# Optimization experiments

Measured on AMD Instinct MI355X. Metric: run time of the kernel, lower is better.

The kernel has to match this reference:

```python
import jax, jax.numpy as jnp
import numpy as np

B, SEQ, D = 2, 1024, 768
E, H = 8, 3072          # num_experts, expert hidden (mlp_ratio=4)
CAPACITY = 2            # k = CAPACITY * num_tokens


def setup_inputs() -> dict:
    key = jax.random.key(0)
    ks = jax.random.split(key, 6)
    x = jax.random.normal(ks[0], (B, SEQ, D), dtype=jnp.float32)
    gate_weight = jax.random.normal(ks[1], (E, D), dtype=jnp.float32) * 0.006
    w1 = jax.random.normal(ks[2], (E, D, H), dtype=jnp.float32) * (1.0 / np.sqrt(D))
    b1 = jnp.zeros((E, H), dtype=jnp.float32)
    w2 = jax.random.normal(ks[3], (E, H, D), dtype=jnp.float32) * (1.0 / np.sqrt(H))
    b2 = jnp.zeros((E, D), dtype=jnp.float32)
    return {"x": x, "gate_weight": gate_weight, "w1": w1, "b1": b1, "w2": w2, "b2": b2}


def reference(x, gate_weight, w1, b1, w2, b2):
    Bb, s, d = x.shape
    xf = x.reshape(-1, d)                     # [S, D]
    S = xf.shape[0]
    k = S * CAPACITY
    logits = xf @ gate_weight.T               # [S, E]
    scores = jax.nn.softmax(logits, axis=-1).T  # [E, S]
    # flattened top-k over all (expert, token) pairs -> sparse gate matrix
    vals, idx = jax.lax.top_k(scores.reshape(-1), k)
    gate = jnp.zeros((E * S,), dtype=x.dtype).at[idx].add(vals).reshape(E, S)
    # expert MLPs (GELU-tanh) applied per expert; zero gate entries kill
    # non-routed (expert, token) pairs -> same math as gather/MLP/scatter.
    h = jax.nn.gelu(jnp.einsum('sd,edh->esh', xf, w1) + b1[:, None, :], approximate=True)
    out = jnp.einsum('esh,ehd->esd', h, w2) + b2[:, None, :]   # [E, S, D]
    y = jnp.einsum('es,esd->sd', gate, out)    # weighted combine + sum over experts
    return y.reshape(Bb, s, d)
```

## Files before the change

kernel.cpp:

```cpp
#include <hip/hip_runtime.h>
#include <math.h>

#define S_TOK 2048
#define NEXP  8
#define DDIM  768
#define HDIM  3072
#define KSEL  4096

typedef __attribute__((ext_vector_type(8))) short short8;
typedef __attribute__((ext_vector_type(4))) float f32x4;

__device__ __forceinline__ unsigned short f2bf(float f) {
  unsigned u = __float_as_uint(f);
  u += 0x7fffu + ((u >> 16) & 1u);
  return (unsigned short)(u >> 16);
}

__device__ __forceinline__ float gelu_fast(float v) {
  float u = 0.7978845608028654f * (v + 0.044715f * v * v * v);
  float t = __expf(-2.0f * fabsf(u));
  float th = (1.0f - t) / (1.0f + t);
  th = copysignf(th, u);
  return 0.5f * v * (1.0f + th);
}

__global__ __launch_bounds__(256) void zero_kernel(float* __restrict__ p, int n) {
  int i = blockIdx.x * 256 + threadIdx.x;
  if (i < n) p[i] = 0.f;
}

__global__ __launch_bounds__(256) void convx_kernel(const float* __restrict__ x,
                                                    short* __restrict__ xb) {
  int i = (blockIdx.x * 256 + threadIdx.x) * 8;
  float4 a = *(const float4*)(x + i);
  float4 b = *(const float4*)(x + i + 4);
  short8 v;
  v[0] = (short)f2bf(a.x); v[1] = (short)f2bf(a.y);
  v[2] = (short)f2bf(a.z); v[3] = (short)f2bf(a.w);
  v[4] = (short)f2bf(b.x); v[5] = (short)f2bf(b.y);
  v[6] = (short)f2bf(b.z); v[7] = (short)f2bf(b.w);
  *(short8*)(xb + i) = v;
}

__global__ __launch_bounds__(256) void gate_kernel(
    const float* __restrict__ x, const float* __restrict__ gw,
    float* __restrict__ scores)
{
  int tid  = threadIdx.x;
  int lane = tid & 63;
  int wid  = tid >> 6;
  int token = blockIdx.x * 4 + wid;
  const float* xr = x + (size_t)token * DDIM;

  float acc[NEXP];
#pragma unroll
  for (int e = 0; e < NEXP; ++e) acc[e] = 0.f;

  for (int d = lane; d < DDIM; d += 64) {
    float xv = xr[d];
#pragma unroll
    for (int e = 0; e < NEXP; ++e) acc[e] += xv * gw[e * DDIM + d];
  }
#pragma unroll
  for (int e = 0; e < NEXP; ++e) {
    for (int off = 32; off; off >>= 1) acc[e] += __shfl_down(acc[e], off, 64);
  }
  if (lane == 0) {
    float m = acc[0];
#pragma unroll
    for (int e = 1; e < NEXP; ++e) m = fmaxf(m, acc[e]);
    float p[NEXP], s = 0.f;
#pragma unroll
    for (int e = 0; e < NEXP; ++e) { p[e] = expf(acc[e] - m); s += p[e]; }
    float inv = 1.0f / s;
#pragma unroll
    for (int e = 0; e < NEXP; ++e) scores[e * S_TOK + token] = p[e] * inv;
  }
}

__device__ unsigned block_scan_excl(unsigned v, volatile unsigned* wsum) {
  int tid = threadIdx.x, lane = tid & 63, wid = tid >> 6;
  __syncthreads();
  unsigned x = v;
#pragma unroll
  for (int off = 1; off < 64; off <<= 1) {
    unsigned t = __shfl_up(x, off, 64);
    if (lane >= off) x += t;
  }
  if (lane == 63) wsum[wid] = x;
  __syncthreads();
  if (tid < 64) {
    unsigned w = (lane < 16) ? wsum[lane] : 0u;
#pragma unroll
    for (int off = 1; off < 16; off <<= 1) {
      unsigned t = __shfl_up(w, off, 64);
      if (lane >= off) w += t;
    }
    if (lane < 16) wsum[lane] = w;
  }
  __syncthreads();
  unsigned woff = (wid > 0) ? wsum[wid - 1] : 0u;
  return woff + (x - v);
}

__global__ __launch_bounds__(1024) void select_kernel(
    const float* __restrict__ scores,
    int* __restrict__ tokenlist, float* __restrict__ slotgate,
    int* __restrict__ offsets)
{
  __shared__ unsigned cnt;
  __shared__ unsigned wsum[16];
  int tid = threadIdx.x;
  int base = tid * 16;

  float sv[16]; unsigned key[16];
#pragma unroll
  for (int j = 0; j < 16; ++j) {
    sv[j] = scores[base + j];
    key[j] = __float_as_uint(sv[j]);
  }

  unsigned lo = 0, hi = 0x3F800000u;
  while (lo < hi) {
    unsigned mid = lo + ((hi - lo + 1) >> 1);
    if (tid == 0) cnt = 0;
    __syncthreads();
    unsigned c = 0;
#pragma unroll
    for (int j = 0; j < 16; ++j) c += (key[j] >= mid) ? 1u : 0u;
    for (int off = 32; off; off >>= 1) c += __shfl_down(c, off, 64);
    if ((tid & 63) == 0) atomicAdd(&cnt, c);
    __syncthreads();
    unsigned tot = cnt;
    __syncthreads();
    if (tot >= (unsigned)KSEL) lo = mid; else hi = mid - 1;
  }
  unsigned V = lo;

  if (tid == 0) cnt = 0;
  __syncthreads();
  {
    unsigned c = 0;
#pragma unroll
    for (int j = 0; j < 16; ++j) c += (key[j] > V) ? 1u : 0u;
    for (int off = 32; off; off >>= 1) c += __shfl_down(c, off, 64);
    if ((tid & 63) == 0) atomicAdd(&cnt, c);
  }
  __syncthreads();
  int need = KSEL - (int)cnt;
  __syncthreads();

  unsigned tloc = 0;
#pragma unroll
  for (int j = 0; j < 16; ++j) tloc += (key[j] == V) ? 1u : 0u;
  unsigned texcl = block_scan_excl(tloc, wsum);

  unsigned selmask = 0, sloc = 0, trun = texcl;
#pragma unroll
  for (int j = 0; j < 16; ++j) {
    bool f;
    if (key[j] > V) f = true;
    else if (key[j] == V) { f = ((int)trun < need); ++trun; }
    else f = false;
    if (f) { selmask |= (1u << j); ++sloc; }
  }
  unsigned sexcl = block_scan_excl(sloc, wsum);

  if ((tid & 127) == 0) offsets[tid >> 7] = (int)sexcl;
  if (tid == 0) offsets[NEXP] = KSEL;

  unsigned p = sexcl;
#pragma unroll
  for (int j = 0; j < 16; ++j) {
    int i = base + j;
    if (selmask & (1u << j)) {
      tokenlist[p] = i & (S_TOK - 1);
      slotgate[p] = sv[j];
      ++p;
    }
  }
}

template <int MODE>
__global__ __launch_bounds__(256) void moe_mfma(
    const short* __restrict__ Abase, const float* __restrict__ W,
    const float* __restrict__ bias, void* __restrict__ outp,
    const int* __restrict__ offsets, const int* __restrict__ tokenlist,
    const float* __restrict__ slotgate)
{
  const int e = (int)blockIdx.x;
  const int K = (MODE == 1) ? DDIM : HDIM;
  const int N = (MODE == 1) ? HDIM : DDIM;
  const int tile  = (MODE == 1) ? (int)blockIdx.z : ((int)blockIdx.z >> 2);
  const int split = (MODE == 1) ? 0 : ((int)blockIdx.z & 3);
  const int klen  = 768;
  const int kb = split * klen;

  const int r0 = offsets[e];
  const int rows = offsets[e + 1] - r0;
  const int rowbase = tile << 7;
  if (rowbase >= rows) return;
  int vr = rows - rowbase; if (vr > 128) vr = 128;
  const int colbase = (int)blockIdx.y << 7;

  __shared__ short As[128 * 40];
  __shared__ short Bb[128 * 40];

  const int tid = threadIdx.x;
  const int lane = tid & 63;
  const int wid = tid >> 6;
  const int wr = (wid >> 1) << 6;
  const int wc = (wid & 1) << 6;
  const int l15 = lane & 15;
  const int lq = lane >> 4;

  const int ar = tid >> 1;
  const int ak = (tid & 1) << 4;
  const short* arow;
  {
    int cr = (ar < vr) ? ar : (vr - 1);
    if (MODE == 1) arow = Abase + (size_t)tokenlist[r0 + rowbase + cr] * DDIM;
    else           arow = Abase + (size_t)(r0 + rowbase + cr) * HDIM + kb;
  }
  const int bn = tid & 127;
  const int bk = (tid >> 7) << 4;
  const float* wcol = W + (size_t)e * K * N + colbase + bn;

  f32x4 acc[4][4];
#pragma unroll
  for (int i = 0; i < 4; ++i)
#pragma unroll
    for (int j = 0; j < 4; ++j) acc[i][j] = (f32x4){0.f, 0.f, 0.f, 0.f};

  short8 av0, av1;
  float bwA[16], bwB[16];
  {
    const short* ap = arow + ak;
    av0 = *(const short8*)(ap);
    av1 = *(const short8*)(ap + 8);
    const float* wpA = wcol + (size_t)(kb + bk) * N;
    const float* wpB = wcol + (size_t)(kb + 32 + bk) * N;
#pragma unroll
    for (int j = 0; j < 16; ++j) bwA[j] = wpA[(size_t)j * N];
#pragma unroll
    for (int j = 0; j < 16; ++j) bwB[j] = wpB[(size_t)j * N];
  }

#define WRITE_LDS(BW)                                            \
  {                                                              \
    *(short8*)&As[ar * 40 + ak] = av0;                           \
    *(short8*)&As[ar * 40 + ak + 8] = av1;                       \
    short8 b0, b1;                                               \
    _Pragma("unroll")                                            \
    for (int m = 0; m < 8; ++m) {                                \
      b0[m] = (short)f2bf(BW[m]);                                \
      b1[m] = (short)f2bf(BW[m + 8]);                            \
    }                                                            \
    *(short8*)&Bb[bn * 40 + bk] = b0;                            \
    *(short8*)&Bb[bn * 40 + bk + 8] = b1;                        \
  }

#define LOAD_A(KN)                                               \
  {                                                              \
    const short* ap = arow + (KN) + ak;                          \
    av0 = *(const short8*)(ap);                                  \
    av1 = *(const short8*)(ap + 8);                              \
  }

#define LOAD_B(BW, KN)                                           \
  {                                                              \
    const float* wp = wcol + (size_t)(kb + (KN) + bk) * N;       \
    _Pragma("unroll")                                            \
    for (int j = 0; j < 16; ++j) BW[j] = wp[(size_t)j * N];      \
  }

#define FRAG_MFMA()                                              \
  {                                                              \
    short8 af[4], bfr[4];                                        \
    _Pragma("unroll")                                            \
    for (int i = 0; i < 4; ++i)                                  \
      af[i] = *(const short8*)&As[(wr + i * 16 + l15) * 40 + lq * 8]; \
    _Pragma("unroll")                                            \
    for (int j = 0; j < 4; ++j)                                  \
      bfr[j] = *(const short8*)&Bb[(wc + j * 16 + l15) * 40 + lq * 8]; \
    _Pragma("unroll")                                            \
    for (int i = 0; i < 4; ++i)                                  \
      _Pragma("unroll")                                          \
      for (int j = 0; j < 4; ++j)                                \
        acc[i][j] = __builtin_amdgcn_mfma_f32_16x16x32_bf16(af[i], bfr[j], acc[i][j], 0, 0, 0); \
  }

#pragma unroll 1
  for (int k0 = 0; k0 < klen; k0 += 64) {
    __syncthreads();
    WRITE_LDS(bwA);
    __syncthreads();
    LOAD_A(k0 + 32);
    { int kn = k0 + 64; if (kn >= klen) kn = k0; LOAD_B(bwA, kn); }
    FRAG_MFMA();
    __syncthreads();
    WRITE_LDS(bwB);
    __syncthreads();
    { int kn = k0 + 64; if (kn >= klen) kn = k0; LOAD_A(kn); }
    { int kn = k0 + 96; if (kn >= klen) kn = k0; LOAD_B(bwB, kn); }
    FRAG_MFMA();
  }

  if (MODE == 1) {
    short* hb = (short*)outp;
    const float* bp = bias + (size_t)e * N + colbase;
#pragma unroll
    for (int i = 0; i < 4; ++i) {
      int rb = wr + i * 16 + lq * 4;
#pragma unroll
      for (int j = 0; j < 4; ++j) {
        int col = wc + j * 16 + l15;
        float bvv = bp[col];
#pragma unroll
        for (int p = 0; p < 4; ++p) {
          int r = rb + p;
          if (r < vr)
            hb[(size_t)(r0 + rowbase + r) * HDIM + colbase + col] =
                (short)f2bf(gelu_fast(acc[i][j][p] + bvv));
        }
      }
    }
  } else {
    float* y = (float*)outp;
    const float* bp = bias + (size_t)e * N + colbase;
#pragma unroll
    for (int i = 0; i < 4; ++i) {
      int rb = wr + i * 16 + lq * 4;
#pragma unroll
      for (int p = 0; p < 4; ++p) {
        int r = rb + p;
        if (r < vr) {
          int gi = r0 + rowbase + r;
          float g = slotgate[gi];
          float* yrow = y + (size_t)tokenlist[gi] * N + colbase;
#pragma unroll
          for (int j = 0; j < 4; ++j) {
            int col = wc + j * 16 + l15;
            float v = acc[i][j][p] + (split == 0 ? bp[col] : 0.f);
            atomicAdd(&yrow[col], g * v);
          }
        }
      }
    }
  }
}

extern "C" void kernel_launch(void* const* d_in, const int* in_sizes, int n_in,
                              void* d_out, int out_size, void* d_ws, size_t ws_size,
                              hipStream_t stream) {
  const float* x  = (const float*)d_in[0];
  const float* gw = (const float*)d_in[1];
  const float* w1 = (const float*)d_in[2];
  const float* b1 = (const float*)d_in[3];
  const float* w2 = (const float*)d_in[4];
  const float* b2 = (const float*)d_in[5];
  float* y = (float*)d_out;

  char* ws = (char*)d_ws;
  float* scores    = (float*)(ws);
  int*   tokenlist = (int*)(ws + (64 << 10));
  float* slotgate  = (float*)(ws + (80 << 10));
  int*   offsets   = (int*)(ws + (96 << 10));
  short* xbf       = (short*)(ws + (128 << 10));
  short* hbuf      = (short*)(ws + (128 << 10) + (size_t)S_TOK * DDIM * 2);

  zero_kernel<<<(out_size + 255) / 256, 256, 0, stream>>>(y, out_size);
  convx_kernel<<<S_TOK * DDIM / 2048, 256, 0, stream>>>(x, xbf);
  gate_kernel<<<S_TOK / 4, 256, 0, stream>>>(x, gw, scores);
  select_kernel<<<1, 1024, 0, stream>>>(scores, tokenlist, slotgate, offsets);

  dim3 g1(NEXP, HDIM / 128, 16);
  moe_mfma<1><<<g1, 256, 0, stream>>>(xbf, w1, b1, hbuf, offsets, tokenlist, slotgate);
  dim3 g2(NEXP, DDIM / 128, 64);
  moe_mfma<2><<<g2, 256, 0, stream>>>(hbuf, w2, b2, y, offsets, tokenlist, slotgate);
}
```

Measured before the change: 208.2 us.

## Coalesce weight loads with transposed LDS reads and replace atomics with combine pass

Weight tiles are now read as contiguous float4 rows along N rather than strided column gathers. They are stored k-major in LDS and fed to MFMA through ds_read_b64_tr_b16 transposed reads, with the k-step reduced to 32 and a single register buffer. The second GEMM's split-K drops from 4 to 2 and writes partial results to a workspace buffer instead of issuing atomicAdds into y. A new combine kernel uses a posmap produced by the selection kernel to gather and gate-weight those partials, which also removes the zeroing kernel. This trades atomic contention and strided global loads for an extra kernel launch and more intermediate memory traffic.

```diff
diff --git a/kernel.cpp b/kernel.cpp
--- a/kernel.cpp
+++ b/kernel.cpp
@@ -9,6 +9,7 @@
 
 typedef __attribute__((ext_vector_type(8))) short short8;
 typedef __attribute__((ext_vector_type(4))) float f32x4;
+typedef __attribute__((ext_vector_type(2))) unsigned int u32x2;
 
 __device__ __forceinline__ unsigned short f2bf(float f) {
   unsigned u = __float_as_uint(f);
@@ -22,11 +23,6 @@
   float th = (1.0f - t) / (1.0f + t);
   th = copysignf(th, u);
   return 0.5f * v * (1.0f + th);
-}
-
-__global__ __launch_bounds__(256) void zero_kernel(float* __restrict__ p, int n) {
-  int i = blockIdx.x * 256 + threadIdx.x;
-  if (i < n) p[i] = 0.f;
 }
 
 __global__ __launch_bounds__(256) void convx_kernel(const float* __restrict__ x,
@@ -106,7 +102,7 @@
 __global__ __launch_bounds__(1024) void select_kernel(
     const float* __restrict__ scores,
     int* __restrict__ tokenlist, float* __restrict__ slotgate,
-    int* __restrict__ offsets)
+    int* __restrict__ offsets, int* __restrict__ posmap)
 {
   __shared__ unsigned cnt;
   __shared__ unsigned wsum[16];
@@ -174,9 +170,12 @@
   for (int j = 0; j < 16; ++j) {
     int i = base + j;
     if (selmask & (1u << j)) {
+      posmap[i] = (int)p;
       tokenlist[p] = i & (S_TOK - 1);
       slotgate[p] = sv[j];
       ++p;
+    } else {
+      posmap[i] = -1;
     }
   }
 }
@@ -185,15 +184,14 @@
 __global__ __launch_bounds__(256) void moe_mfma(
     const short* __restrict__ Abase, const float* __restrict__ W,
     const float* __restrict__ bias, void* __restrict__ outp,
-    const int* __restrict__ offsets, const int* __restrict__ tokenlist,
-    const float* __restrict__ slotgate)
+    const int* __restrict__ offsets, const int* __restrict__ tokenlist)
 {
   const int e = (int)blockIdx.x;
   const int K = (MODE == 1) ? DDIM : HDIM;
   const int N = (MODE == 1) ? HDIM : DDIM;
-  const int tile  = (MODE == 1) ? (int)blockIdx.z : ((int)blockIdx.z >> 2);
-  const int split = (MODE == 1) ? 0 : ((int)blockIdx.z & 3);
-  const int klen  = 768;
+  const int tile  = (MODE == 1) ? (int)blockIdx.z : ((int)blockIdx.z >> 1);
+  const int split = (MODE == 1) ? 0 : ((int)blockIdx.z & 1);
+  const int klen  = (MODE == 1) ? DDIM : (HDIM / 2);
   const int kb = split * klen;
 
   const int r0 = offsets[e];
@@ -204,7 +202,8 @@
   const int colbase = (int)blockIdx.y << 7;
 
   __shared__ short As[128 * 40];
-  __shared__ short Bb[128 * 40];
+  __shared__ __align__(16) short Bs[32 * 128];
+  const unsigned bs_lds = (unsigned)(uintptr_t)&Bs[0];
 
   const int tid = threadIdx.x;
   const int lane = tid & 63;
@@ -222,9 +221,11 @@
     if (MODE == 1) arow = Abase + (size_t)tokenlist[r0 + rowbase + cr] * DDIM;
     else           arow = Abase + (size_t)(r0 + rowbase + cr) * HDIM + kb;
   }
-  const int bn = tid & 127;
-  const int bk = (tid >> 7) << 4;
-  const float* wcol = W + (size_t)e * K * N + colbase + bn;
+
+  const int sk = tid >> 3;
+  const int g8 = tid & 7;
+  const float* wsrc = W + (size_t)e * K * N + (size_t)kb * N + colbase + g8 * 16;
+  short* bwr = (short*)Bs + ((((sk >> 2) << 3) + g8) << 6) + ((sk & 3) << 4);
 
   f32x4 acc[4][4];
 #pragma unroll
@@ -232,78 +233,57 @@
 #pragma unroll
     for (int j = 0; j < 4; ++j) acc[i][j] = (f32x4){0.f, 0.f, 0.f, 0.f};
 
-  short8 av0, av1;
-  float bwA[16], bwB[16];
+  short8 avA0, avA1;
+  float4 bw[4];
   {
-    const short* ap = arow + ak;
-    av0 = *(const short8*)(ap);
-    av1 = *(const short8*)(ap + 8);
-    const float* wpA = wcol + (size_t)(kb + bk) * N;
-    const float* wpB = wcol + (size_t)(kb + 32 + bk) * N;
-#pragma unroll
-    for (int j = 0; j < 16; ++j) bwA[j] = wpA[(size_t)j * N];
-#pragma unroll
-    for (int j = 0; j < 16; ++j) bwB[j] = wpB[(size_t)j * N];
-  }
-
-#define WRITE_LDS(BW)                                            \
-  {                                                              \
-    *(short8*)&As[ar * 40 + ak] = av0;                           \
-    *(short8*)&As[ar * 40 + ak + 8] = av1;                       \
-    short8 b0, b1;                                               \
-    _Pragma("unroll")                                            \
-    for (int m = 0; m < 8; ++m) {                                \
-      b0[m] = (short)f2bf(BW[m]);                                \
-      b1[m] = (short)f2bf(BW[m + 8]);                            \
-    }                                                            \
-    *(short8*)&Bb[bn * 40 + bk] = b0;                            \
-    *(short8*)&Bb[bn * 40 + bk + 8] = b1;                        \
-  }
-
-#define LOAD_A(KN)                                               \
-  {                                                              \
-    const short* ap = arow + (KN) + ak;                          \
-    av0 = *(const short8*)(ap);                                  \
-    av1 = *(const short8*)(ap + 8);                              \
-  }
-
-#define LOAD_B(BW, KN)                                           \
-  {                                                              \
-    const float* wp = wcol + (size_t)(kb + (KN) + bk) * N;       \
-    _Pragma("unroll")                                            \
-    for (int j = 0; j < 16; ++j) BW[j] = wp[(size_t)j * N];      \
-  }
-
-#define FRAG_MFMA()                                              \
-  {                                                              \
-    short8 af[4], bfr[4];                                        \
-    _Pragma("unroll")                                            \
-    for (int i = 0; i < 4; ++i)                                  \
-      af[i] = *(const short8*)&As[(wr + i * 16 + l15) * 40 + lq * 8]; \
-    _Pragma("unroll")                                            \
-    for (int j = 0; j < 4; ++j)                                  \
-      bfr[j] = *(const short8*)&Bb[(wc + j * 16 + l15) * 40 + lq * 8]; \
-    _Pragma("unroll")                                            \
-    for (int i = 0; i < 4; ++i)                                  \
-      _Pragma("unroll")                                          \
-      for (int j = 0; j < 4; ++j)                                \
-        acc[i][j] = __builtin_amdgcn_mfma_f32_16x16x32_bf16(af[i], bfr[j], acc[i][j], 0, 0, 0); \
+    avA0 = *(const short8*)(arow + ak);
+    avA1 = *(const short8*)(arow + ak + 8);
+    const float* wp = wsrc + (size_t)sk * N;
+#pragma unroll
+    for (int q = 0; q < 4; ++q) bw[q] = *(const float4*)(wp + 4 * q);
   }
 
 #pragma unroll 1
-  for (int k0 = 0; k0 < klen; k0 += 64) {
-    __syncthreads();
-    WRITE_LDS(bwA);
-    __syncthreads();
-    LOAD_A(k0 + 32);
-    { int kn = k0 + 64; if (kn >= klen) kn = k0; LOAD_B(bwA, kn); }
-    FRAG_MFMA();
-    __syncthreads();
-    WRITE_LDS(bwB);
-    __syncthreads();
-    { int kn = k0 + 64; if (kn >= klen) kn = k0; LOAD_A(kn); }
-    { int kn = k0 + 96; if (kn >= klen) kn = k0; LOAD_B(bwB, kn); }
-    FRAG_MFMA();
+  for (int k0 = 0; k0 < klen; k0 += 32) {
+    __syncthreads();
+    *(short8*)&As[ar * 40 + ak] = avA0;
+    *(short8*)&As[ar * 40 + ak + 8] = avA1;
+#pragma unroll
+    for (int q = 0; q < 4; ++q) {
+      u32x2 pk;
+      pk[0] = (unsigned)f2bf(bw[q].x) | ((unsigned)f2bf(bw[q].y) << 16);
+      pk[1] = (unsigned)f2bf(bw[q].z) | ((unsigned)f2bf(bw[q].w) << 16);
+      *(u32x2*)(bwr + 4 * q) = pk;
+    }
+    __syncthreads();
+    if (k0 + 32 < klen) {
+      avA0 = *(const short8*)(arow + k0 + 32 + ak);
+      avA1 = *(const short8*)(arow + k0 + 32 + ak + 8);
+      const float* wp = wsrc + (size_t)(k0 + 32 + sk) * N;
+#pragma unroll
+      for (int q = 0; q < 4; ++q) bw[q] = *(const float4*)(wp + 4 * q);
+    }
+    short8 af[4], bfr[4];
+#pragma unroll
+    for (int i = 0; i < 4; ++i)
+      af[i] = *(const short8*)&As[(wr + i * 16 + l15) * 40 + lq * 8];
+#pragma unroll
+    for (int j = 0; j < 4; ++j) {
+      unsigned off = bs_lds + ((unsigned)((lq << 4) + (wc >> 4) + j) << 7) +
+                     ((unsigned)l15 << 3);
+      union { short8 s; u32x2 u[2]; } fb;
+      asm volatile("ds_read_b64_tr_b16 %0, %2 offset:0\n\t"
+                   "ds_read_b64_tr_b16 %1, %2 offset:1024"
+                   : "=&v"(fb.u[0]), "=&v"(fb.u[1]) : "v"(off));
+      bfr[j] = fb.s;
+    }
+    asm volatile("s_waitcnt lgkmcnt(0)" ::: "memory");
+    __builtin_amdgcn_sched_barrier(0);
+#pragma unroll
+    for (int i = 0; i < 4; ++i)
+#pragma unroll
+      for (int j = 0; j < 4; ++j)
+        acc[i][j] = __builtin_amdgcn_mfma_f32_16x16x32_bf16(af[i], bfr[j], acc[i][j], 0, 0, 0);
   }
 
   if (MODE == 1) {
@@ -326,7 +306,7 @@
       }
     }
   } else {
-    float* y = (float*)outp;
+    float* ob = (float*)outp + (size_t)split * KSEL * DDIM;
     const float* bp = bias + (size_t)e * N + colbase;
 #pragma unroll
     for (int i = 0; i < 4; ++i) {
@@ -335,19 +315,41 @@
       for (int p = 0; p < 4; ++p) {
         int r = rb + p;
         if (r < vr) {
-          int gi = r0 + rowbase + r;
-          float g = slotgate[gi];
-          float* yrow = y + (size_t)tokenlist[gi] * N + colbase;
+          float* orow = ob + (size_t)(r0 + rowbase + r) * DDIM + colbase;
 #pragma unroll
           for (int j = 0; j < 4; ++j) {
             int col = wc + j * 16 + l15;
-            float v = acc[i][j][p] + (split == 0 ? bp[col] : 0.f);
-            atomicAdd(&yrow[col], g * v);
+            orow[col] = acc[i][j][p] + (split == 0 ? bp[col] : 0.f);
           }
         }
       }
     }
   }
+}
+
+__global__ __launch_bounds__(256) void combine_kernel(
+    const float* __restrict__ outbuf, const int* __restrict__ posmap,
+    const float* __restrict__ slotgate, float* __restrict__ y)
+{
+  int s = blockIdx.x;
+  int tid = threadIdx.x;
+  float a0 = 0.f, a1 = 0.f, a2 = 0.f;
+#pragma unroll
+  for (int e = 0; e < NEXP; ++e) {
+    int p = posmap[e * S_TOK + s];
+    if (p >= 0) {
+      float g = slotgate[p];
+      const float* o0 = outbuf + (size_t)p * DDIM;
+      const float* o1 = outbuf + ((size_t)KSEL + p) * DDIM;
+      a0 += g * (o0[tid] + o1[tid]);
+      a1 += g * (o0[tid + 256] + o1[tid + 256]);
+      a2 += g * (o0[tid + 512] + o1[tid + 512]);
+    }
+  }
+  float* yr = y + (size_t)s * DDIM;
+  yr[tid] = a0;
+  yr[tid + 256] = a1;
+  yr[tid + 512] = a2;
 }
 
 extern "C" void kernel_launch(void* const* d_in, const int* in_sizes, int n_in,
@@ -366,16 +368,20 @@
   int*   tokenlist = (int*)(ws + (64 << 10));
   float* slotgate  = (float*)(ws + (80 << 10));
   int*   offsets   = (int*)(ws + (96 << 10));
-  short* xbf       = (short*)(ws + (128 << 10));
-  short* hbuf      = (short*)(ws + (128 << 10) + (size_t)S_TOK * DDIM * 2);
-
-  zero_kernel<<<(out_size + 255) / 256, 256, 0, stream>>>(y, out_size);
+  int*   posmap    = (int*)(ws + (128 << 10));
+  short* xbf       = (short*)(ws + (192 << 10));
+  short* hbuf      = (short*)(ws + (192 << 10) + (size_t)S_TOK * DDIM * 2);
+  float* outbuf    = (float*)(ws + (192 << 10) + (size_t)S_TOK * DDIM * 2
+                                  + (size_t)KSEL * HDIM * 2);
+
   convx_kernel<<<S_TOK * DDIM / 2048, 256, 0, stream>>>(x, xbf);
   gate_kernel<<<S_TOK / 4, 256, 0, stream>>>(x, gw, scores);
-  select_kernel<<<1, 1024, 0, stream>>>(scores, tokenlist, slotgate, offsets);
+  select_kernel<<<1, 1024, 0, stream>>>(scores, tokenlist, slotgate, offsets, posmap);
 
   dim3 g1(NEXP, HDIM / 128, 16);
-  moe_mfma<1><<<g1, 256, 0, stream>>>(xbf, w1, b1, hbuf, offsets, tokenlist, slotgate);
-  dim3 g2(NEXP, DDIM / 128, 64);
-  moe_mfma<2><<<g2, 256, 0, stream>>>(hbuf, w2, b2, y, offsets, tokenlist, slotgate);
-}
+  moe_mfma<1><<<g1, 256, 0, stream>>>(xbf, w1, b1, hbuf, offsets, tokenlist);
+  dim3 g2(NEXP, DDIM / 128, 32);
+  moe_mfma<2><<<g2, 256, 0, stream>>>(hbuf, w2, b2, outbuf, offsets, tokenlist);
+
+  combine_kernel<<<S_TOK, 256, 0, stream>>>(outbuf, posmap, slotgate, y);
+}
```

New measurement: 196.1 us. 1.06x faster.

## Double-buffer LDS and load weights row-major with transposing LDS reads

Applied to the files above, without the earlier changes.

Weight tiles are now read with coalesced float4 loads along the N dimension and stored k-major in LDS. The B fragments are then fetched with ds_read_b64_tr_b16 transpose reads instead of strided scalar global loads. A and B tiles are double-buffered in LDS so the next tile's write and prefetch overlap the current MFMA step, which cuts the four barriers per 64-k chunk to two. The cost is more LDS use, inline asm that depends on gfx950 transpose-read semantics, and manual waitcnt and sched_barrier handling.

```diff
diff --git a/kernel.cpp b/kernel.cpp
--- a/kernel.cpp
+++ b/kernel.cpp
@@ -9,6 +9,7 @@
 
 typedef __attribute__((ext_vector_type(8))) short short8;
 typedef __attribute__((ext_vector_type(4))) float f32x4;
+typedef __attribute__((ext_vector_type(2))) unsigned int u32x2;
 
 __device__ __forceinline__ unsigned short f2bf(float f) {
   unsigned u = __float_as_uint(f);
@@ -203,8 +204,12 @@
   int vr = rows - rowbase; if (vr > 128) vr = 128;
   const int colbase = (int)blockIdx.y << 7;
 
-  __shared__ short As[128 * 40];
-  __shared__ short Bb[128 * 40];
+  __shared__ short As0[128 * 40];
+  __shared__ short As1[128 * 40];
+  __shared__ __align__(16) short Bs0[32 * 128];
+  __shared__ __align__(16) short Bs1[32 * 128];
+  const unsigned bs0_lds = (unsigned)(uintptr_t)&Bs0[0];
+  const unsigned bs1_lds = (unsigned)(uintptr_t)&Bs1[0];
 
   const int tid = threadIdx.x;
   const int lane = tid & 63;
@@ -222,9 +227,11 @@
     if (MODE == 1) arow = Abase + (size_t)tokenlist[r0 + rowbase + cr] * DDIM;
     else           arow = Abase + (size_t)(r0 + rowbase + cr) * HDIM + kb;
   }
-  const int bn = tid & 127;
-  const int bk = (tid >> 7) << 4;
-  const float* wcol = W + (size_t)e * K * N + colbase + bn;
+
+  const int sk = tid >> 3;
+  const int g8 = tid & 7;
+  const float* wsrc = W + (size_t)e * K * N + (size_t)kb * N + colbase + g8 * 16;
+  const int bwoff = ((((sk >> 2) << 3) + g8) << 6) + ((sk & 3) << 4);
 
   f32x4 acc[4][4];
 #pragma unroll
@@ -232,78 +239,70 @@
 #pragma unroll
     for (int j = 0; j < 4; ++j) acc[i][j] = (f32x4){0.f, 0.f, 0.f, 0.f};
 
-  short8 av0, av1;
-  float bwA[16], bwB[16];
-  {
-    const short* ap = arow + ak;
-    av0 = *(const short8*)(ap);
-    av1 = *(const short8*)(ap + 8);
-    const float* wpA = wcol + (size_t)(kb + bk) * N;
-    const float* wpB = wcol + (size_t)(kb + 32 + bk) * N;
-#pragma unroll
-    for (int j = 0; j < 16; ++j) bwA[j] = wpA[(size_t)j * N];
-#pragma unroll
-    for (int j = 0; j < 16; ++j) bwB[j] = wpB[(size_t)j * N];
-  }
-
-#define WRITE_LDS(BW)                                            \
+  short8 avA0, avA1;
+  float4 bw[4];
+
+#define LOAD_AB(KN)                                              \
   {                                                              \
-    *(short8*)&As[ar * 40 + ak] = av0;                           \
-    *(short8*)&As[ar * 40 + ak + 8] = av1;                       \
-    short8 b0, b1;                                               \
-    _Pragma("unroll")                                            \
-    for (int m = 0; m < 8; ++m) {                                \
-      b0[m] = (short)f2bf(BW[m]);                                \
-      b1[m] = (short)f2bf(BW[m + 8]);                            \
+    avA0 = *(const short8*)(arow + (KN) + ak);                   \
+    avA1 = *(const short8*)(arow + (KN) + ak + 8);               \
+    const float* wp = wsrc + (size_t)((KN) + sk) * N;            \
+    _Pragma("unroll")                                            \
+    for (int q = 0; q < 4; ++q) bw[q] = *(const float4*)(wp + 4 * q); \
+  }
+
+#define WRITE_LDS(AS, BS)                                        \
+  {                                                              \
+    *(short8*)&AS[ar * 40 + ak] = avA0;                          \
+    *(short8*)&AS[ar * 40 + ak + 8] = avA1;                      \
+    _Pragma("unroll")                                            \
+    for (int q = 0; q < 4; ++q) {                                \
+      u32x2 pk;                                                  \
+      pk[0] = (unsigned)f2bf(bw[q].x) | ((unsigned)f2bf(bw[q].y) << 16); \
+      pk[1] = (unsigned)f2bf(bw[q].z) | ((unsigned)f2bf(bw[q].w) << 16); \
+      *(u32x2*)((short*)BS + bwoff + 4 * q) = pk;                \
     }                                                            \
-    *(short8*)&Bb[bn * 40 + bk] = b0;                            \
-    *(short8*)&Bb[bn * 40 + bk + 8] = b1;                        \
-  }
-
-#define LOAD_A(KN)                                               \
-  {                                                              \
-    const short* ap = arow + (KN) + ak;                          \
-    av0 = *(const short8*)(ap);                                  \
-    av1 = *(const short8*)(ap + 8);                              \
-  }
-
-#define LOAD_B(BW, KN)                                           \
-  {                                                              \
-    const float* wp = wcol + (size_t)(kb + (KN) + bk) * N;       \
-    _Pragma("unroll")                                            \
-    for (int j = 0; j < 16; ++j) BW[j] = wp[(size_t)j * N];      \
-  }
-
-#define FRAG_MFMA()                                              \
+  }
+
+#define KSTEP(RA, RBLDS, WA, WB, KC)                             \
   {                                                              \
     short8 af[4], bfr[4];                                        \
     _Pragma("unroll")                                            \
     for (int i = 0; i < 4; ++i)                                  \
-      af[i] = *(const short8*)&As[(wr + i * 16 + l15) * 40 + lq * 8]; \
-    _Pragma("unroll")                                            \
-    for (int j = 0; j < 4; ++j)                                  \
-      bfr[j] = *(const short8*)&Bb[(wc + j * 16 + l15) * 40 + lq * 8]; \
+      af[i] = *(const short8*)&RA[(wr + i * 16 + l15) * 40 + lq * 8]; \
+    _Pragma("unroll")                                            \
+    for (int j = 0; j < 4; ++j) {                                \
+      unsigned off = (RBLDS) + ((unsigned)((lq << 4) + (wc >> 4) + j) << 7) + \
+                     ((unsigned)l15 << 3);                       \
+      union { short8 s; u32x2 u[2]; } fb;                        \
+      asm volatile("ds_read_b64_tr_b16 %0, %2 offset:0\n\t"      \
+                   "ds_read_b64_tr_b16 %1, %2 offset:1024"       \
+                   : "=&v"(fb.u[0]), "=&v"(fb.u[1]) : "v"(off)); \
+      bfr[j] = fb.s;                                             \
+    }                                                            \
+    if ((KC) + 32 < klen) {                                      \
+      WRITE_LDS(WA, WB);                                         \
+      if ((KC) + 64 < klen) LOAD_AB((KC) + 64);                  \
+    }                                                            \
+    asm volatile("s_waitcnt lgkmcnt(0)" ::: "memory");           \
+    __builtin_amdgcn_sched_barrier(0);                           \
     _Pragma("unroll")                                            \
     for (int i = 0; i < 4; ++i)                                  \
       _Pragma("unroll")                                          \
       for (int j = 0; j < 4; ++j)                                \
         acc[i][j] = __builtin_amdgcn_mfma_f32_16x16x32_bf16(af[i], bfr[j], acc[i][j], 0, 0, 0); \
-  }
+    __syncthreads();                                             \
+  }
+
+  LOAD_AB(0);
+  WRITE_LDS(As0, Bs0);
+  LOAD_AB(32);
+  __syncthreads();
 
 #pragma unroll 1
   for (int k0 = 0; k0 < klen; k0 += 64) {
-    __syncthreads();
-    WRITE_LDS(bwA);
-    __syncthreads();
-    LOAD_A(k0 + 32);
-    { int kn = k0 + 64; if (kn >= klen) kn = k0; LOAD_B(bwA, kn); }
-    FRAG_MFMA();
-    __syncthreads();
-    WRITE_LDS(bwB);
-    __syncthreads();
-    { int kn = k0 + 64; if (kn >= klen) kn = k0; LOAD_A(kn); }
-    { int kn = k0 + 96; if (kn >= klen) kn = k0; LOAD_B(bwB, kn); }
-    FRAG_MFMA();
+    KSTEP(As0, bs0_lds, As1, Bs1, k0);
+    KSTEP(As1, bs1_lds, As0, Bs0, k0 + 32);
   }
 
   if (MODE == 1) {
```

New measurement: 210.4 us. No clear change (+1.0%).
